# Optimization experiments

Measured on AMD Instinct MI355X. Metric: run time of the kernel, lower is better.

Reference implementation:

```python
import jax, jax.numpy as jnp
import numpy as np

MARGIN = 0.3
FAMILY_TABLE = jnp.array([0, 1, 2, 1, 3, 3], dtype=jnp.int32)  # num_classes == 6
_BIG = 1e9  # finite sentinel (avoids inf*0 NaNs under autodiff)
_EPS = 1e-12  # F.normalize eps


def setup_inputs() -> dict:
    key = jax.random.key(0)
    k1, k2 = jax.random.split(key)
    B, D = 8192, 64
    embeddings = jax.random.normal(k1, (B, D), dtype=jnp.float32)
    labels = jax.random.randint(k2, (B,), 0, 6, dtype=jnp.int64)
    return {"embeddings": embeddings, "labels": labels}


def reference(embeddings, labels):
    B = embeddings.shape[0]
    # fam[i] = family_table[labels[i]]; labels are always < len(table) here,
    # so no -1 entries occur (matches original semantics for in-range labels).
    fam = jnp.take(FAMILY_TABLE, labels)  # [B]

    # L2-normalize rows (F.normalize with eps clamp)
    norm = jnp.maximum(jnp.linalg.norm(embeddings, axis=-1, keepdims=True), _EPS)
    emb_norm = embeddings / norm

    # cosine distance matrix [B, B]
    dist = 1.0 - emb_norm @ emb_norm.T

    same = (fam[:, None] == fam[None, :]) & (~jnp.eye(B, dtype=bool))  # [B,B]
    diff = fam[:, None] != fam[None, :]                                 # [B,B]

    d_pos = jnp.max(jnp.where(same, dist, -_BIG), axis=1)  # hardest positive
    d_neg = jnp.min(jnp.where(diff, dist, _BIG), axis=1)   # hardest negative

    valid = same.any(axis=1) & diff.any(axis=1)  # rows contributing to loss
    per_row = jnp.where(valid, jax.nn.relu(d_pos - d_neg + MARGIN), 0.0)

    count = jnp.sum(valid.astype(jnp.float32))
    return jnp.sum(per_row) / jnp.maximum(count, 1.0)
```

## Files before the change

kernel.cpp:

```cpp
#include <hip/hip_runtime.h>
#include <math.h>

#define MARGIN 0.3f
#define NJ 64
#define NPAIR 4

typedef short bf16x8 __attribute__((ext_vector_type(8)));
typedef float f32x4 __attribute__((ext_vector_type(4)));

__device__ __forceinline__ unsigned short f2bf_rne(float x) {
    unsigned b = __float_as_uint(x);
    unsigned r = b + 0x7FFFu + ((b >> 16) & 1u);
    return (unsigned short)(r >> 16);
}
__device__ __forceinline__ int fam_of(int lbl) { return (0xF64 >> (2 * lbl)) & 3; }

__global__ __launch_bounds__(1024) void sort_kernel(const int* __restrict__ labels,
                                                    int* __restrict__ posOf,
                                                    unsigned char* __restrict__ famSorted,
                                                    int* __restrict__ famLoHi, int B) {
    const int t = threadIdx.x;
    const int lane = t & 63, w = t >> 6;
    int lc[4] = {0, 0, 0, 0};
    int lf[8], lr[8];
#pragma unroll
    for (int j = 0; j < 8; j++) {
        int f = fam_of(labels[t * 8 + j]);
        lf[j] = f; lr[j] = lc[f]++;
    }
    int inc[4];
#pragma unroll
    for (int f = 0; f < 4; f++) {
        int v = lc[f];
#pragma unroll
        for (int o = 1; o < 64; o <<= 1) {
            int u = __shfl_up(v, o, 64);
            if (lane >= o) v += u;
        }
        inc[f] = v;
    }
    __shared__ int waveTot[16][4], waveBase[16][4], famBase[4], famTotS[4];
    if (lane == 63)
#pragma unroll
        for (int f = 0; f < 4; f++) waveTot[w][f] = inc[f];
    __syncthreads();
    if (t < 64) {
        int f = t >> 4, ww = t & 15;
        int v = waveTot[ww][f];
#pragma unroll
        for (int o = 1; o < 16; o <<= 1) {
            int u = __shfl_up(v, o, 64);
            if ((t & 15) >= o) v += u;
        }
        waveBase[ww][f] = v - waveTot[ww][f];
        if (ww == 15) famTotS[f] = v;
    }
    __syncthreads();
    if (t == 0) {
        int b = 0;
#pragma unroll
        for (int f = 0; f < 4; f++) {
            famBase[f] = b; famLoHi[f] = b; b += famTotS[f]; famLoHi[4 + f] = b;
        }
    }
    __syncthreads();
    int base[4];
#pragma unroll
    for (int f = 0; f < 4; f++) base[f] = famBase[f] + waveBase[w][f] + (inc[f] - lc[f]);
#pragma unroll
    for (int j = 0; j < 8; j++) {
        int pos = base[lf[j]] + lr[j];
        posOf[t * 8 + j] = pos;
        famSorted[pos] = (unsigned char)lf[j];
    }
}

__global__ __launch_bounds__(256) void normpack_kernel(const float* __restrict__ emb,
                                                       const int* __restrict__ posOf,
                                                       short* __restrict__ pack, int B) {
    const int lane = threadIdx.x & 63;
    const int wid  = threadIdx.x >> 6;
    const int row  = blockIdx.x * 4 + wid;
    float x = emb[(size_t)row * 64 + lane];
    float ss = x * x;
#pragma unroll
    for (int o = 32; o > 0; o >>= 1) ss += __shfl_xor(ss, o, 64);
    float n = fmaxf(sqrtf(ss), 1e-12f);
    unsigned short h = f2bf_rne(x / n);
    int pos = posOf[row];
    size_t idx = (size_t)(pos >> 4) * 1024 + (size_t)(lane >> 3) * 128 + (size_t)(pos & 15) * 8 + (lane & 7);
    pack[idx] = (short)h;
}

__global__ __launch_bounds__(256) void gemm_minmax_kernel(
    const short* __restrict__ pack,
    const unsigned char* __restrict__ famSorted, const int* __restrict__ famLoHi,
    float* __restrict__ pMin, float* __restrict__ pMax, int B) {
    const int lane = threadIdx.x & 63;
    const int wid  = threadIdx.x >> 6;
    const int g = lane >> 4;
    const int c = lane & 15;
    const int rowBase = blockIdx.x * 256 + wid * 64;
    const int aStrip0 = rowBase >> 4;

    bf16x8 aH[4][2];
#pragma unroll
    for (int s = 0; s < 4; s++) {
        const short* pA = pack + (size_t)(aStrip0 + s) * 1024;
        aH[s][0] = *(const bf16x8*)(pA + lane * 8);
        aH[s][1] = *(const bf16x8*)(pA + 512 + lane * 8);
    }

    int sLo[4], sHi[4], sUni[4];
#pragma unroll
    for (int s = 0; s < 4; s++) {
        int f0  = famSorted[rowBase + s * 16];
        int f15 = famSorted[rowBase + s * 16 + 15];
        sUni[s] = __builtin_amdgcn_readfirstlane((f0 == f15) ? 1 : 0);
        sLo[s]  = __builtin_amdgcn_readfirstlane(famLoHi[f0]);
        sHi[s]  = __builtin_amdgcn_readfirstlane(famLoHi[4 + f0]);
    }

    const f32x4 zq = {0.f, 0.f, 0.f, 0.f};
    float mn[4] = {1e30f, 1e30f, 1e30f, 1e30f};
    float mx[4] = {-1e30f, -1e30f, -1e30f, -1e30f};

    const int jChunk0 = blockIdx.y * 128;
    const int jStrip0 = jChunk0 >> 4;
    const short* pBbase = pack + (size_t)jStrip0 * 1024;

#pragma unroll
    for (int jp = 0; jp < NPAIR; jp++) {
        const int j0 = jChunk0 + jp * 32;
        const short* pB0 = pBbase + (size_t)(2 * jp) * 1024;
        const short* pB1 = pB0 + 1024;
        bf16x8 b0h0 = *(const bf16x8*)(pB0 + lane * 8);
        bf16x8 b0h1 = *(const bf16x8*)(pB0 + 512 + lane * 8);
        bf16x8 b1h0 = *(const bf16x8*)(pB1 + lane * 8);
        bf16x8 b1h1 = *(const bf16x8*)(pB1 + 512 + lane * 8);

#pragma unroll
        for (int s = 0; s < 4; s++) {
            f32x4 accA, accB;
            accA = __builtin_amdgcn_mfma_f32_16x16x32_bf16(b0h0, aH[s][0], zq, 0, 0, 0);
            accB = __builtin_amdgcn_mfma_f32_16x16x32_bf16(b1h0, aH[s][0], zq, 0, 0, 0);
            accA = __builtin_amdgcn_mfma_f32_16x16x32_bf16(b0h1, aH[s][1], accA, 0, 0, 0);
            accB = __builtin_amdgcn_mfma_f32_16x16x32_bf16(b1h1, aH[s][1], accB, 0, 0, 0);

            if (sUni[s] && j0 >= sLo[s] && j0 + 32 <= sHi[s]) {
                float a01 = fminf(accA[0], accA[1]), a23 = fminf(accA[2], accA[3]);
                float b01 = fminf(accB[0], accB[1]), b23 = fminf(accB[2], accB[3]);
                mn[s] = fminf(mn[s], fminf(fminf(a01, a23), fminf(b01, b23)));
            } else if (sUni[s] && (j0 >= sHi[s] || j0 + 32 <= sLo[s])) {
                float a01 = fmaxf(accA[0], accA[1]), a23 = fmaxf(accA[2], accA[3]);
                float b01 = fmaxf(accB[0], accB[1]), b23 = fmaxf(accB[2], accB[3]);
                mx[s] = fmaxf(mx[s], fmaxf(fmaxf(a01, a23), fmaxf(b01, b23)));
            } else {
                int fi = famSorted[rowBase + s * 16 + c];
                unsigned fjA = *(const unsigned*)(famSorted + j0 + g * 4);
                unsigned fjB = *(const unsigned*)(famSorted + j0 + 16 + g * 4);
#pragma unroll
                for (int r = 0; r < 4; r++) {
                    bool sameA = ((int)((fjA >> (8 * r)) & 255u) == fi);
                    bool sameB = ((int)((fjB >> (8 * r)) & 255u) == fi);
                    mn[s] = fminf(mn[s], sameA ? accA[r] : 1e30f);
                    mx[s] = fmaxf(mx[s], sameA ? -1e30f : accA[r]);
                    mn[s] = fminf(mn[s], sameB ? accB[r] : 1e30f);
                    mx[s] = fmaxf(mx[s], sameB ? -1e30f : accB[r]);
                }
            }
        }
    }

#pragma unroll
    for (int s = 0; s < 4; s++) {
        float mnv = mn[s], mxv = mx[s];
        mnv = fminf(mnv, __shfl_xor(mnv, 16, 64));
        mxv = fmaxf(mxv, __shfl_xor(mxv, 16, 64));
        mnv = fminf(mnv, __shfl_xor(mnv, 32, 64));
        mxv = fmaxf(mxv, __shfl_xor(mxv, 32, 64));
        if (g == 0) {
            int row = rowBase + s * 16 + c;
            pMin[(size_t)blockIdx.y * B + row] = mnv;
            pMax[(size_t)blockIdx.y * B + row] = mxv;
        }
    }
}

__global__ __launch_bounds__(256) void rowloss_kernel(const float* __restrict__ pMin,
                                                      const float* __restrict__ pMax,
                                                      float* __restrict__ partial, int B) {
    const int row = blockIdx.x * 256 + threadIdx.x;
    float mn = 1e30f, mx = -1e30f;
#pragma unroll 8
    for (int cn = 0; cn < NJ; cn++) {
        mn = fminf(mn, pMin[(size_t)cn * B + row]);
        mx = fmaxf(mx, pMax[(size_t)cn * B + row]);
    }
    float sum = 0.f, cnt = 0.f;
    if (mn < 1e29f && mx > -1e29f) {
        sum = fmaxf(mx - mn + MARGIN, 0.f);
        cnt = 1.f;
    }
#pragma unroll
    for (int o = 32; o > 0; o >>= 1) {
        sum += __shfl_xor(sum, o, 64);
        cnt += __shfl_xor(cnt, o, 64);
    }
    __shared__ float sS[4], sC[4];
    const int lane = threadIdx.x & 63, w = threadIdx.x >> 6;
    if (lane == 0) { sS[w] = sum; sC[w] = cnt; }
    __syncthreads();
    if (threadIdx.x == 0) {
        partial[blockIdx.x]      = sS[0] + sS[1] + sS[2] + sS[3];
        partial[64 + blockIdx.x] = sC[0] + sC[1] + sC[2] + sC[3];
    }
}

__global__ void final_kernel(const float* __restrict__ partial, float* __restrict__ out, int nb) {
    if (threadIdx.x == 0) {
        float S = 0.f, C = 0.f;
        for (int i = 0; i < nb; i++) { S += partial[i]; C += partial[64 + i]; }
        out[0] = S / fmaxf(C, 1.f);
    }
}

extern "C" void kernel_launch(void* const* d_in, const int* in_sizes, int n_in,
                              void* d_out, int out_size, void* d_ws, size_t ws_size,
                              hipStream_t stream) {
    const float* emb    = (const float*)d_in[0];
    const int*   labels = (const int*)d_in[1];
    const int B = in_sizes[1];

    char* base = (char*)d_ws;
    size_t off = 0;
    auto alloc = [&](size_t bytes) -> char* {
        char* p = base + off;
        off = (off + bytes + 255) & ~(size_t)255;
        return p;
    };
    int*           posOf     = (int*)alloc((size_t)B * 4);
    unsigned char* famSorted = (unsigned char*)alloc((size_t)B);
    int*           famLoHi   = (int*)alloc(32);
    short*         pack      = (short*)alloc((size_t)B * 64 * 2);
    float*         pMin      = (float*)alloc((size_t)NJ * B * 4);
    float*         pMax      = (float*)alloc((size_t)NJ * B * 4);
    float*         partial   = (float*)alloc(128 * 4);

    sort_kernel<<<1, 1024, 0, stream>>>(labels, posOf, famSorted, famLoHi, B);
    normpack_kernel<<<B / 4, 256, 0, stream>>>(emb, posOf, pack, B);
    dim3 g3(B / 256, NJ);
    gemm_minmax_kernel<<<g3, 256, 0, stream>>>(pack, famSorted, famLoHi, pMin, pMax, B);
    rowloss_kernel<<<B / 256, 256, 0, stream>>>(pMin, pMax, partial, B);
    final_kernel<<<1, 64, 0, stream>>>(partial, (float*)d_out, B / 256);
}
```

Measured before the change: 33.78 us.

## Stage B tiles in LDS via direct loads, widen column chunk, fuse final reduction

The GEMM kernel now covers 256 columns per block instead of 128, halving the number of column chunks. It stages the shared B strip into LDS once per block with global_load_lds, so the four waves no longer each read B from global memory. The final single-thread kernel is folded into the row-loss kernel using an atomic counter and last-block reduction, which removes one launch. In exchange each block uses 32 KB of LDS and a barrier, which may reduce occupancy and adds a synchronisation point before compute starts.

```diff
diff --git a/kernel.cpp b/kernel.cpp
--- a/kernel.cpp
+++ b/kernel.cpp
@@ -2,11 +2,14 @@
 #include <math.h>
 
 #define MARGIN 0.3f
-#define NJ 64
-#define NPAIR 4
+#define NJ 32
+#define NPAIR 8
 
 typedef short bf16x8 __attribute__((ext_vector_type(8)));
 typedef float f32x4 __attribute__((ext_vector_type(4)));
+typedef unsigned int u32;
+typedef const __attribute__((address_space(1))) u32* gp_t;
+typedef __attribute__((address_space(3))) u32* lp_t;
 
 __device__ __forceinline__ unsigned short f2bf_rne(float x) {
     unsigned b = __float_as_uint(x);
@@ -18,9 +21,11 @@
 __global__ __launch_bounds__(1024) void sort_kernel(const int* __restrict__ labels,
                                                     int* __restrict__ posOf,
                                                     unsigned char* __restrict__ famSorted,
-                                                    int* __restrict__ famLoHi, int B) {
+                                                    int* __restrict__ famLoHi,
+                                                    unsigned* __restrict__ counter, int B) {
     const int t = threadIdx.x;
     const int lane = t & 63, w = t >> 6;
+    if (t == 0) *counter = 0;
     int lc[4] = {0, 0, 0, 0};
     int lf[8], lr[8];
 #pragma unroll
@@ -96,12 +101,16 @@
     const short* __restrict__ pack,
     const unsigned char* __restrict__ famSorted, const int* __restrict__ famLoHi,
     float* __restrict__ pMin, float* __restrict__ pMax, int B) {
+    __shared__ short ldsB[16384];
+
     const int lane = threadIdx.x & 63;
     const int wid  = threadIdx.x >> 6;
     const int g = lane >> 4;
     const int c = lane & 15;
     const int rowBase = blockIdx.x * 256 + wid * 64;
     const int aStrip0 = rowBase >> 4;
+    const int jChunk0 = blockIdx.y * 256;
+    const int jStrip0 = jChunk0 >> 4;
 
     bf16x8 aH[4][2];
 #pragma unroll
@@ -109,6 +118,16 @@
         const short* pA = pack + (size_t)(aStrip0 + s) * 1024;
         aH[s][0] = *(const bf16x8*)(pA + lane * 8);
         aH[s][1] = *(const bf16x8*)(pA + 512 + lane * 8);
+    }
+
+    {
+        const char* src = (const char*)(pack + (size_t)jStrip0 * 1024);
+#pragma unroll
+        for (int i = 0; i < 8; i++) {
+            int off = wid * 8192 + i * 1024;
+            __builtin_amdgcn_global_load_lds((gp_t)(src + off + lane * 16),
+                                             (lp_t)((char*)ldsB + off), 16, 0, 0);
+        }
     }
 
     int sLo[4], sHi[4], sUni[4];
@@ -125,14 +144,12 @@
     float mn[4] = {1e30f, 1e30f, 1e30f, 1e30f};
     float mx[4] = {-1e30f, -1e30f, -1e30f, -1e30f};
 
-    const int jChunk0 = blockIdx.y * 128;
-    const int jStrip0 = jChunk0 >> 4;
-    const short* pBbase = pack + (size_t)jStrip0 * 1024;
+    __syncthreads();
 
 #pragma unroll
     for (int jp = 0; jp < NPAIR; jp++) {
         const int j0 = jChunk0 + jp * 32;
-        const short* pB0 = pBbase + (size_t)(2 * jp) * 1024;
+        const short* pB0 = ldsB + (size_t)(2 * jp) * 1024;
         const short* pB1 = pB0 + 1024;
         bf16x8 b0h0 = *(const bf16x8*)(pB0 + lane * 8);
         bf16x8 b0h1 = *(const bf16x8*)(pB0 + 512 + lane * 8);
@@ -187,9 +204,12 @@
     }
 }
 
-__global__ __launch_bounds__(256) void rowloss_kernel(const float* __restrict__ pMin,
-                                                      const float* __restrict__ pMax,
-                                                      float* __restrict__ partial, int B) {
+__global__ __launch_bounds__(256) void rowloss_final_kernel(const float* __restrict__ pMin,
+                                                            const float* __restrict__ pMax,
+                                                            float* __restrict__ partial,
+                                                            unsigned* __restrict__ counter,
+                                                            float* __restrict__ out, int B) {
+    const int nb = B / 256;
     const int row = blockIdx.x * 256 + threadIdx.x;
     float mn = 1e30f, mx = -1e30f;
 #pragma unroll 8
@@ -214,14 +234,14 @@
     if (threadIdx.x == 0) {
         partial[blockIdx.x]      = sS[0] + sS[1] + sS[2] + sS[3];
         partial[64 + blockIdx.x] = sC[0] + sC[1] + sC[2] + sC[3];
-    }
-}
-
-__global__ void final_kernel(const float* __restrict__ partial, float* __restrict__ out, int nb) {
-    if (threadIdx.x == 0) {
-        float S = 0.f, C = 0.f;
-        for (int i = 0; i < nb; i++) { S += partial[i]; C += partial[64 + i]; }
-        out[0] = S / fmaxf(C, 1.f);
+        __threadfence();
+        unsigned done = atomicAdd(counter, 1u);
+        if (done == (unsigned)(nb - 1)) {
+            __threadfence();
+            float S = 0.f, C = 0.f;
+            for (int i = 0; i < nb; i++) { S += partial[i]; C += partial[64 + i]; }
+            out[0] = S / fmaxf(C, 1.f);
+        }
     }
 }
 
@@ -242,15 +262,16 @@
     int*           posOf     = (int*)alloc((size_t)B * 4);
     unsigned char* famSorted = (unsigned char*)alloc((size_t)B);
     int*           famLoHi   = (int*)alloc(32);
+    unsigned*      counter   = (unsigned*)alloc(64);
     short*         pack      = (short*)alloc((size_t)B * 64 * 2);
     float*         pMin      = (float*)alloc((size_t)NJ * B * 4);
     float*         pMax      = (float*)alloc((size_t)NJ * B * 4);
     float*         partial   = (float*)alloc(128 * 4);
 
-    sort_kernel<<<1, 1024, 0, stream>>>(labels, posOf, famSorted, famLoHi, B);
+    sort_kernel<<<1, 1024, 0, stream>>>(labels, posOf, famSorted, famLoHi, counter, B);
     normpack_kernel<<<B / 4, 256, 0, stream>>>(emb, posOf, pack, B);
     dim3 g3(B / 256, NJ);
     gemm_minmax_kernel<<<g3, 256, 0, stream>>>(pack, famSorted, famLoHi, pMin, pMax, B);
-    rowloss_kernel<<<B / 256, 256, 0, stream>>>(pMin, pMax, partial, B);
-    final_kernel<<<1, 64, 0, stream>>>(partial, (float*)d_out, B / 256);
-}
+    rowloss_final_kernel<<<B / 256, 256, 0, stream>>>(pMin, pMax, partial, counter,
+                                                      (float*)d_out, B);
+}
```

Result: no change. 33.26 us (-1.5%).
